# Optimization experiments

Hardware: AMD Instinct MI355X
Metric: run time of the kernel (lower is better)

The kernel has to match this reference:

```python
import jax, jax.numpy as jnp
import numpy as np

V_MIN = -10.0
V_MAX = 10.0
N_ATOMS = 101
LN_EPS = 1e-5

B = 131072
N_OBS = 60
N_ACT = 20
H = 256


def _layer_norm(x, g, b):
    mu = jnp.mean(x, axis=-1, keepdims=True)
    var = jnp.mean(jnp.square(x - mu), axis=-1, keepdims=True)
    return (x - mu) * jax.lax.rsqrt(var + LN_EPS) * g + b


def _mlp(x, W1, b1, g1, be1, W2, b2, g2, be2, W3, b3, g3, be3, W4, b4):
    h = jax.nn.silu(_layer_norm(x @ W1 + b1, g1, be1))
    h = jax.nn.silu(_layer_norm(h @ W2 + b2, g2, be2))
    h = jax.nn.silu(_layer_norm(h @ W3 + b3, g3, be3))
    return h @ W4 + b4  # [B, N_ATOMS] logits


def setup_inputs() -> dict:
    key = jax.random.key(0)
    ks = jax.random.split(key, 10)
    s = 0.05
    return {
        'obs': jax.random.normal(ks[0], (B, N_OBS), jnp.float32),
        'actions': jax.random.normal(ks[1], (B, N_ACT), jnp.float32),
        'rewards': jax.random.normal(ks[2], (B,), jnp.float32),
        'bootstrap': jax.random.uniform(ks[3], (B,), jnp.float32),
        'discount': jax.random.uniform(ks[4], (B,), jnp.float32, 0.95, 0.99),
        'q_support': jnp.linspace(V_MIN, V_MAX, N_ATOMS, dtype=jnp.float32),
        'W1': jax.random.normal(ks[5], (N_OBS + N_ACT, H), jnp.float32) * s,
        'b1': jnp.zeros((H,), jnp.float32),
        'g1': jnp.ones((H,), jnp.float32),
        'be1': jnp.zeros((H,), jnp.float32),
        'W2': jax.random.normal(ks[6], (H, H // 2), jnp.float32) * s,
        'b2': jnp.zeros((H // 2,), jnp.float32),
        'g2': jnp.ones((H // 2,), jnp.float32),
        'be2': jnp.zeros((H // 2,), jnp.float32),
        'W3': jax.random.normal(ks[7], (H // 2, H // 4), jnp.float32) * s,
        'b3': jnp.zeros((H // 4,), jnp.float32),
        'g3': jnp.ones((H // 4,), jnp.float32),
        'be3': jnp.zeros((H // 4,), jnp.float32),
        'W4': jax.random.normal(ks[8], (H // 4, N_ATOMS), jnp.float32) * s,
        'b4': jnp.zeros((N_ATOMS,), jnp.float32),
    }


def reference(obs, actions, rewards, bootstrap, discount, q_support,
              W1, b1, g1, be1, W2, b2, g2, be2, W3, b3, g3, be3, W4, b4):
    batch = rewards.shape[0]
    delta_z = (V_MAX - V_MIN) / (N_ATOMS - 1)
    # Bellman target support: [B, N_ATOMS]
    target_z = rewards[:, None] + bootstrap[:, None] * discount[:, None] * q_support
    target_z = jnp.clip(target_z, V_MIN, V_MAX)
    b = (target_z - V_MIN) / delta_z
    li = jnp.floor(b).astype(jnp.int32)
    ui = jnp.ceil(b).astype(jnp.int32)
    is_int = ui == li
    lower_mask = is_int & (li > 0)
    upper_mask = is_int & (li == 0)
    li = jnp.where(lower_mask, li - 1, li)
    ui = jnp.where(upper_mask, ui + 1, ui)
    lf = li.astype(b.dtype)
    uf = ui.astype(b.dtype)

    x = jnp.concatenate([obs, actions], axis=-1)
    logits = _mlp(x, W1, b1, g1, be1, W2, b2, g2, be2, W3, b3, g3, be3, W4, b4)
    next_dist = jax.nn.softmax(logits, axis=1)

    size = batch * N_ATOMS
    offset = (jnp.arange(batch, dtype=jnp.int32) * N_ATOMS)[:, None]
    l_idx = jnp.clip((li + offset).reshape(-1), 0, size - 1)
    u_idx = jnp.clip((ui + offset).reshape(-1), 0, size - 1)
    lw = (next_dist * (uf - b)).reshape(-1)
    uw = (next_dist * (b - lf)).reshape(-1)
    proj = jnp.zeros((size,), next_dist.dtype).at[l_idx].add(lw).at[u_idx].add(uw)
    return proj.reshape(batch, N_ATOMS)
```

## Files before the change

### kernel.cpp

```cpp
#include <hip/hip_runtime.h>
#include <math.h>

typedef __bf16 bf16x8 __attribute__((ext_vector_type(8)));
typedef float f32x4 __attribute__((ext_vector_type(4)));

__global__ void conv_weights(const float* __restrict__ W1, const float* __restrict__ W2,
                             const float* __restrict__ W3, const float* __restrict__ W4,
                             __bf16* __restrict__ ws)
{
  const int f = blockIdx.x;
  const int lane = threadIdx.x;
  int f0, ntot, Ksrc, Nsrc, off;
  const float* W;
  if (f < 48)       { f0 = f;       ntot = 16; Ksrc = 80;  Nsrc = 256; W = W1; off = 0; }
  else if (f < 112) { f0 = f - 48;  ntot = 8;  Ksrc = 256; Nsrc = 128; W = W2; off = 24576; }
  else if (f < 128) { f0 = f - 112; ntot = 4;  Ksrc = 128; Nsrc = 64;  W = W3; off = 57344; }
  else              { f0 = f - 128; ntot = 8;  Ksrc = 64;  Nsrc = 101; W = W4; off = 65536; }
  const int kt = f0 / ntot, nt = f0 % ntot;
  const int q = lane >> 4, c = lane & 15;
  const int n = nt * 16 + c;
  bf16x8 v;
#pragma unroll
  for (int j = 0; j < 8; ++j) {
    const int k = kt * 32 + q * 8 + j;
    const float x = (k < Ksrc && n < Nsrc) ? W[k * Nsrc + n] : 0.f;
    v[j] = (__bf16)x;
  }
  ((bf16x8*)(ws + off))[f0 * 64 + lane] = v;
}


template<int KT, int NTW, int NTOT, int SIN, int SOUT>
__device__ __forceinline__ void layer(
    const __bf16* __restrict__ aIn, __bf16* __restrict__ aOut,
    const bf16x8* __restrict__ Bfrags, int n0t,
    const float* __restrict__ bias, const float* __restrict__ g,
    const float* __restrict__ be,
    float* __restrict__ lnS, float* __restrict__ lnS2,
    float* __restrict__ muS, float* __restrict__ rsS,
    int t, int lane)
{
  const int q = lane >> 4, c = lane & 15;
  const int wv = t >> 6;
  bf16x8 Bf[KT][NTW];
#pragma unroll
  for (int kt = 0; kt < KT; ++kt)
#pragma unroll
    for (int nt = 0; nt < NTW; ++nt)
      Bf[kt][nt] = Bfrags[(kt * NTOT + n0t + nt) * 64 + lane];
  f32x4 acc[2][NTW];
#pragma unroll
  for (int nt = 0; nt < NTW; ++nt) {
    const float bb = bias[(n0t + nt) * 16 + c];
    f32x4 v = {bb, bb, bb, bb};
    acc[0][nt] = v;
    acc[1][nt] = v;
  }
#pragma unroll
  for (int mt = 0; mt < 2; ++mt)
#pragma unroll
    for (int kt = 0; kt < KT; ++kt) {
      const bf16x8 A = *(const bf16x8*)(aIn + (mt * 16 + c) * SIN + kt * 32 + q * 8);
#pragma unroll
      for (int nt = 0; nt < NTW; ++nt)
        acc[mt][nt] = __builtin_amdgcn_mfma_f32_16x16x32_bf16(A, Bf[kt][nt], acc[mt][nt], 0, 0, 0);
    }
#pragma unroll
  for (int mt = 0; mt < 2; ++mt)
#pragma unroll
    for (int r = 0; r < 4; ++r) {
      float s = 0.f, s2 = 0.f;
#pragma unroll
      for (int nt = 0; nt < NTW; ++nt) { const float v = acc[mt][nt][r]; s += v; s2 += v * v; }
      s += __shfl_xor(s, 1); s2 += __shfl_xor(s2, 1);
      s += __shfl_xor(s, 2); s2 += __shfl_xor(s2, 2);
      s += __shfl_xor(s, 4); s2 += __shfl_xor(s2, 4);
      s += __shfl_xor(s, 8); s2 += __shfl_xor(s2, 8);
      if (c == 0) {
        const int row = mt * 16 + 4 * q + r;
        lnS[row * 4 + wv] = s;
        lnS2[row * 4 + wv] = s2;
      }
    }
  __syncthreads();
  if (t < 32) {
    const float s  = lnS[t * 4] + lnS[t * 4 + 1] + lnS[t * 4 + 2] + lnS[t * 4 + 3];
    const float s2 = lnS2[t * 4] + lnS2[t * 4 + 1] + lnS2[t * 4 + 2] + lnS2[t * 4 + 3];
    const float invN = 1.f / (float)(NTOT * 16);
    const float mu = s * invN;
    const float var = s2 * invN - mu * mu;
    muS[t] = mu;
    rsS[t] = rsqrtf(var + 1e-5f);
  }
  __syncthreads();
#pragma unroll
  for (int nt = 0; nt < NTW; ++nt) {
    const int col = (n0t + nt) * 16 + c;
    const float gg = g[col], bb = be[col];
#pragma unroll
    for (int mt = 0; mt < 2; ++mt)
#pragma unroll
      for (int r = 0; r < 4; ++r) {
        const int row = mt * 16 + 4 * q + r;
        float v = (acc[mt][nt][r] - muS[row]) * rsS[row] * gg + bb;
        v = v / (1.f + __expf(-v));
        aOut[row * SOUT + col] = (__bf16)v;
      }
  }
  __syncthreads();
}

__global__ __launch_bounds__(256, 4)
void sacq_mfma(const float* __restrict__ obs,  const float* __restrict__ act,
               const float* __restrict__ rew,  const float* __restrict__ boot,
               const float* __restrict__ disc, const float* __restrict__ qsup,
               const float* __restrict__ b1, const float* __restrict__ g1, const float* __restrict__ be1,
               const float* __restrict__ b2, const float* __restrict__ g2, const float* __restrict__ be2,
               const float* __restrict__ b3, const float* __restrict__ g3, const float* __restrict__ be3,
               const float* __restrict__ b4,
               const __bf16* __restrict__ ws,
               float* __restrict__ out)
{
  __shared__ float smf[7152];
  __bf16* xb = (__bf16*)smf;
  __bf16* h2 = (__bf16*)smf;
  __bf16* h1 = (__bf16*)(smf + 2176);
  __bf16* h3 = (__bf16*)(smf + 2176);
  float* proj = smf + 3328;
  float* lnS  = smf + 6656;
  float* lnS2 = smf + 6784;
  float* muS  = smf + 6912;
  float* rsS  = smf + 6944;
  float* qsL  = smf + 6976;
  float* rwL  = smf + 7080;
  float* bdL  = smf + 7112;

  const int t = threadIdx.x;
  const int lane = t & 63, wv = t >> 6;
  const int q = lane >> 4, c = lane & 15;
  const long row0 = (long)blockIdx.x * 32;

  for (int idx = t; idx < 32 * 60; idx += 256) {
    const int r = idx / 60, cc = idx - r * 60;
    xb[r * 104 + cc] = (__bf16)obs[row0 * 60 + idx];
  }
  for (int idx = t; idx < 32 * 20; idx += 256) {
    const int r = idx / 20, cc = idx - r * 20;
    xb[r * 104 + 60 + cc] = (__bf16)act[row0 * 20 + idx];
  }
  for (int idx = t; idx < 32 * 24; idx += 256) {
    const int r = idx / 24, cc = idx - r * 24;
    xb[r * 104 + 80 + cc] = (__bf16)0.f;
  }
  if (t < 101) qsL[t] = qsup[t];
  if (t >= 128 && t < 160) {
    const int r = t - 128;
    rwL[r] = rew[row0 + r];
    bdL[r] = boot[row0 + r] * disc[row0 + r];
  }
  __syncthreads();

  const bf16x8* wsf = (const bf16x8*)ws;
  layer<3, 4, 16, 104, 264>(xb, h1, wsf + 0,    wv * 4, b1, g1, be1, lnS, lnS2, muS, rsS, t, lane);
  layer<8, 2, 8, 264, 136>(h1, h2, wsf + 3072, wv * 2, b2, g2, be2, lnS, lnS2, muS, rsS, t, lane);
  layer<4, 1, 4, 136, 72>(h2, h3, wsf + 7168,  wv,     b3, g3, be3, lnS, lnS2, muS, rsS, t, lane);

  {
    const int mtw = wv >> 1;
    const int half = wv & 1;
    bf16x8 Bf4[2][4];
#pragma unroll
    for (int kt = 0; kt < 2; ++kt)
#pragma unroll
      for (int nt = 0; nt < 4; ++nt)
        Bf4[kt][nt] = wsf[8192 + (kt * 8 + half * 4 + nt) * 64 + lane];
    f32x4 a4[4];
#pragma unroll
    for (int nt = 0; nt < 4; ++nt) {
      const int col = (half * 4 + nt) * 16 + c;
      const float bb = (col < 101) ? b4[col] : 0.f;
      f32x4 v = {bb, bb, bb, bb};
      a4[nt] = v;
    }
#pragma unroll
    for (int kt = 0; kt < 2; ++kt) {
      const bf16x8 A = *(const bf16x8*)(h3 + (mtw * 16 + c) * 72 + kt * 32 + q * 8);
#pragma unroll
      for (int nt = 0; nt < 4; ++nt)
        a4[nt] = __builtin_amdgcn_mfma_f32_16x16x32_bf16(A, Bf4[kt][nt], a4[nt], 0, 0, 0);
    }
#pragma unroll
    for (int r = 0; r < 4; ++r) {
      float mx = -3.4e38f;
#pragma unroll
      for (int nt = 0; nt < 4; ++nt) {
        const int col = (half * 4 + nt) * 16 + c;
        if (col < 101) mx = fmaxf(mx, a4[nt][r]);
      }
      mx = fmaxf(mx, __shfl_xor(mx, 1));
      mx = fmaxf(mx, __shfl_xor(mx, 2));
      mx = fmaxf(mx, __shfl_xor(mx, 4));
      mx = fmaxf(mx, __shfl_xor(mx, 8));
      if (c == 0) lnS[(mtw * 16 + 4 * q + r) * 2 + half] = mx;
    }
    __syncthreads();
    for (int idx = t; idx < 32 * 104; idx += 256) proj[idx] = 0.f;
#pragma unroll
    for (int r = 0; r < 4; ++r) {
      const int row = mtw * 16 + 4 * q + r;
      const float mxf = fmaxf(lnS[row * 2], lnS[row * 2 + 1]);
      float s = 0.f;
#pragma unroll
      for (int nt = 0; nt < 4; ++nt) {
        const int col = (half * 4 + nt) * 16 + c;
        const float e = (col < 101) ? __expf(a4[nt][r] - mxf) : 0.f;
        a4[nt][r] = e;
        s += e;
      }
      s += __shfl_xor(s, 1);
      s += __shfl_xor(s, 2);
      s += __shfl_xor(s, 4);
      s += __shfl_xor(s, 8);
      if (c == 0) lnS2[row * 2 + half] = s;
    }
    __syncthreads();
#pragma unroll
    for (int r = 0; r < 4; ++r) {
      const int row = mtw * 16 + 4 * q + r;
      const float inv = 1.f / (lnS2[row * 2] + lnS2[row * 2 + 1]);
      const float rw = rwL[row], bd = bdL[row];
#pragma unroll
      for (int nt = 0; nt < 4; ++nt) {
        const int col = (half * 4 + nt) * 16 + c;
        if (col < 101) {
          const float p = a4[nt][r] * inv;
          float tz = rw + bd * qsL[col];
          tz = fminf(fmaxf(tz, -10.f), 10.f);
          const float b_ = (tz + 10.f) / 0.2f;
          const float fl = floorf(b_), cl = ceilf(b_);
          int li = (int)fl, ui = (int)cl;
          if (ui == li) { if (li > 0) --li; else ++ui; }
          atomicAdd(&proj[row * 104 + li], p * ((float)ui - b_));
          atomicAdd(&proj[row * 104 + ui], p * (b_ - (float)li));
        }
      }
    }
    __syncthreads();
  }

  for (int idx = t; idx < 32 * 101; idx += 256) {
    const int r = idx / 101, cc = idx - r * 101;
    out[row0 * 101 + idx] = proj[r * 104 + cc];
  }
}

extern "C" void kernel_launch(void* const* d_in, const int* in_sizes, int n_in,
                              void* d_out, int out_size, void* d_ws, size_t ws_size,
                              hipStream_t stream)
{
  const int B = in_sizes[2];
  __bf16* ws = (__bf16*)d_ws;

  conv_weights<<<dim3(144), dim3(64), 0, stream>>>(
      (const float*)d_in[6], (const float*)d_in[10], (const float*)d_in[14],
      (const float*)d_in[18], ws);

  sacq_mfma<<<dim3(B / 32), dim3(256), 0, stream>>>(
      (const float*)d_in[0],  (const float*)d_in[1],  (const float*)d_in[2],
      (const float*)d_in[3],  (const float*)d_in[4],  (const float*)d_in[5],
      (const float*)d_in[7],  (const float*)d_in[8],  (const float*)d_in[9],
      (const float*)d_in[11], (const float*)d_in[12], (const float*)d_in[13],
      (const float*)d_in[15], (const float*)d_in[16], (const float*)d_in[17],
      (const float*)d_in[19], ws, (float*)d_out);
}
```

Before: 356.8 us.

## Make each wavefront own 16 rows end-to-end, removing block-wide syncs

Restructures the fused MLP+projection kernel so each wavefront handles 16 batch rows through all four layers independently, using private LDS regions and wave-level shuffles for LayerNorm and softmax instead of cross-wave reductions and __syncthreads. Weights are read from global (cache) per MFMA instead of preloaded fragments, inputs are loaded straight into registers, and output is written with vector stores. This removes barrier stalls and cross-wave LDS reductions. In exchange it needs more registers (launch bounds drop to 3 blocks per SIMD), more LDS per block, and heavier weight traffic per wave.

```diff
diff --git a/kernel.cpp b/kernel.cpp
--- a/kernel.cpp
+++ b/kernel.cpp
@@ -8,8 +8,8 @@
                              const float* __restrict__ W3, const float* __restrict__ W4,
                              __bf16* __restrict__ ws)
 {
-  const int f = blockIdx.x;
-  const int lane = threadIdx.x;
+  const int f = blockIdx.x * 4 + (threadIdx.x >> 6);
+  const int lane = threadIdx.x & 63;
   int f0, ntot, Ksrc, Nsrc, off;
   const float* W;
   if (f < 48)       { f0 = f;       ntot = 16; Ksrc = 80;  Nsrc = 256; W = W1; off = 0; }
@@ -30,88 +30,8 @@
 }
 
 
-template<int KT, int NTW, int NTOT, int SIN, int SOUT>
-__device__ __forceinline__ void layer(
-    const __bf16* __restrict__ aIn, __bf16* __restrict__ aOut,
-    const bf16x8* __restrict__ Bfrags, int n0t,
-    const float* __restrict__ bias, const float* __restrict__ g,
-    const float* __restrict__ be,
-    float* __restrict__ lnS, float* __restrict__ lnS2,
-    float* __restrict__ muS, float* __restrict__ rsS,
-    int t, int lane)
-{
-  const int q = lane >> 4, c = lane & 15;
-  const int wv = t >> 6;
-  bf16x8 Bf[KT][NTW];
-#pragma unroll
-  for (int kt = 0; kt < KT; ++kt)
-#pragma unroll
-    for (int nt = 0; nt < NTW; ++nt)
-      Bf[kt][nt] = Bfrags[(kt * NTOT + n0t + nt) * 64 + lane];
-  f32x4 acc[2][NTW];
-#pragma unroll
-  for (int nt = 0; nt < NTW; ++nt) {
-    const float bb = bias[(n0t + nt) * 16 + c];
-    f32x4 v = {bb, bb, bb, bb};
-    acc[0][nt] = v;
-    acc[1][nt] = v;
-  }
-#pragma unroll
-  for (int mt = 0; mt < 2; ++mt)
-#pragma unroll
-    for (int kt = 0; kt < KT; ++kt) {
-      const bf16x8 A = *(const bf16x8*)(aIn + (mt * 16 + c) * SIN + kt * 32 + q * 8);
-#pragma unroll
-      for (int nt = 0; nt < NTW; ++nt)
-        acc[mt][nt] = __builtin_amdgcn_mfma_f32_16x16x32_bf16(A, Bf[kt][nt], acc[mt][nt], 0, 0, 0);
-    }
-#pragma unroll
-  for (int mt = 0; mt < 2; ++mt)
-#pragma unroll
-    for (int r = 0; r < 4; ++r) {
-      float s = 0.f, s2 = 0.f;
-#pragma unroll
-      for (int nt = 0; nt < NTW; ++nt) { const float v = acc[mt][nt][r]; s += v; s2 += v * v; }
-      s += __shfl_xor(s, 1); s2 += __shfl_xor(s2, 1);
-      s += __shfl_xor(s, 2); s2 += __shfl_xor(s2, 2);
-      s += __shfl_xor(s, 4); s2 += __shfl_xor(s2, 4);
-      s += __shfl_xor(s, 8); s2 += __shfl_xor(s2, 8);
-      if (c == 0) {
-        const int row = mt * 16 + 4 * q + r;
-        lnS[row * 4 + wv] = s;
-        lnS2[row * 4 + wv] = s2;
-      }
-    }
-  __syncthreads();
-  if (t < 32) {
-    const float s  = lnS[t * 4] + lnS[t * 4 + 1] + lnS[t * 4 + 2] + lnS[t * 4 + 3];
-    const float s2 = lnS2[t * 4] + lnS2[t * 4 + 1] + lnS2[t * 4 + 2] + lnS2[t * 4 + 3];
-    const float invN = 1.f / (float)(NTOT * 16);
-    const float mu = s * invN;
-    const float var = s2 * invN - mu * mu;
-    muS[t] = mu;
-    rsS[t] = rsqrtf(var + 1e-5f);
-  }
-  __syncthreads();
-#pragma unroll
-  for (int nt = 0; nt < NTW; ++nt) {
-    const int col = (n0t + nt) * 16 + c;
-    const float gg = g[col], bb = be[col];
-#pragma unroll
-    for (int mt = 0; mt < 2; ++mt)
-#pragma unroll
-      for (int r = 0; r < 4; ++r) {
-        const int row = mt * 16 + 4 * q + r;
-        float v = (acc[mt][nt][r] - muS[row]) * rsS[row] * gg + bb;
-        v = v / (1.f + __expf(-v));
-        aOut[row * SOUT + col] = (__bf16)v;
-      }
-  }
-  __syncthreads();
-}
-
-__global__ __launch_bounds__(256, 4)
-void sacq_mfma(const float* __restrict__ obs,  const float* __restrict__ act,
+__global__ __launch_bounds__(256, 3)
+void sacq_wave(const float* __restrict__ obs,  const float* __restrict__ act,
                const float* __restrict__ rew,  const float* __restrict__ boot,
                const float* __restrict__ disc, const float* __restrict__ qsup,
                const float* __restrict__ b1, const float* __restrict__ g1, const float* __restrict__ be1,
@@ -121,136 +41,250 @@
                const __bf16* __restrict__ ws,
                float* __restrict__ out)
 {
-  __shared__ float smf[7152];
-  __bf16* xb = (__bf16*)smf;
-  __bf16* h2 = (__bf16*)smf;
-  __bf16* h1 = (__bf16*)(smf + 2176);
-  __bf16* h3 = (__bf16*)(smf + 2176);
-  float* proj = smf + 3328;
-  float* lnS  = smf + 6656;
-  float* lnS2 = smf + 6784;
-  float* muS  = smf + 6912;
-  float* rsS  = smf + 6944;
-  float* qsL  = smf + 6976;
-  float* rwL  = smf + 7080;
-  float* bdL  = smf + 7112;
-
+  __shared__ float sm[13120];
   const int t = threadIdx.x;
-  const int lane = t & 63, wv = t >> 6;
+  const int wv = t >> 6, lane = t & 63;
   const int q = lane >> 4, c = lane & 15;
-  const long row0 = (long)blockIdx.x * 32;
-
-  for (int idx = t; idx < 32 * 60; idx += 256) {
-    const int r = idx / 60, cc = idx - r * 60;
-    xb[r * 104 + cc] = (__bf16)obs[row0 * 60 + idx];
-  }
-  for (int idx = t; idx < 32 * 20; idx += 256) {
-    const int r = idx / 20, cc = idx - r * 20;
-    xb[r * 104 + 60 + cc] = (__bf16)act[row0 * 20 + idx];
-  }
-  for (int idx = t; idx < 32 * 24; idx += 256) {
-    const int r = idx / 24, cc = idx - r * 24;
-    xb[r * 104 + 80 + cc] = (__bf16)0.f;
-  }
-  if (t < 101) qsL[t] = qsup[t];
-  if (t >= 128 && t < 160) {
-    const int r = t - 128;
-    rwL[r] = rew[row0 + r];
-    bdL[r] = boot[row0 + r] * disc[row0 + r];
-  }
-  __syncthreads();
-
+  float* smw = sm + wv * 3280;
+  __bf16* h1 = (__bf16*)smw;
+  __bf16* h2 = (__bf16*)(smw + 2192);
+  __bf16* h3 = (__bf16*)smw;
+  float*  proj = smw + 576;
+  const int row0w = blockIdx.x * 64 + wv * 16;
   const bf16x8* wsf = (const bf16x8*)ws;
-  layer<3, 4, 16, 104, 264>(xb, h1, wsf + 0,    wv * 4, b1, g1, be1, lnS, lnS2, muS, rsS, t, lane);
-  layer<8, 2, 8, 264, 136>(h1, h2, wsf + 3072, wv * 2, b2, g2, be2, lnS, lnS2, muS, rsS, t, lane);
-  layer<4, 1, 4, 136, 72>(h2, h3, wsf + 7168,  wv,     b3, g3, be3, lnS, lnS2, muS, rsS, t, lane);
-
-  {
-    const int mtw = wv >> 1;
-    const int half = wv & 1;
-    bf16x8 Bf4[2][4];
-#pragma unroll
-    for (int kt = 0; kt < 2; ++kt)
+
+  {
+    bf16x8 A1[3];
+    const float* obsR = obs + (size_t)(row0w + c) * 60;
+    const float* actR = act + (size_t)(row0w + c) * 20;
+#pragma unroll
+    for (int kt = 0; kt < 3; ++kt)
+#pragma unroll
+      for (int j = 0; j < 8; ++j) {
+        const int k = kt * 32 + q * 8 + j;
+        float xv = 0.f;
+        if (k < 60) xv = obsR[k];
+        else if (k < 80) xv = actR[k - 60];
+        A1[kt][j] = (__bf16)xv;
+      }
+    f32x4 acc1[16];
+#pragma unroll
+    for (int nt = 0; nt < 16; ++nt) {
+      const float bb = b1[nt * 16 + c];
+      f32x4 v = {bb, bb, bb, bb};
+      acc1[nt] = v;
+    }
+#pragma unroll
+    for (int kt = 0; kt < 3; ++kt)
+#pragma unroll
+      for (int nt = 0; nt < 16; ++nt)
+        acc1[nt] = __builtin_amdgcn_mfma_f32_16x16x32_bf16(A1[kt], wsf[(kt * 16 + nt) * 64 + lane], acc1[nt], 0, 0, 0);
+
+    float mu[4], rs[4];
+#pragma unroll
+    for (int r = 0; r < 4; ++r) {
+      float s = 0.f, s2 = 0.f;
+#pragma unroll
+      for (int nt = 0; nt < 16; ++nt) { const float v = acc1[nt][r]; s += v; s2 += v * v; }
+      s += __shfl_xor(s, 1); s2 += __shfl_xor(s2, 1);
+      s += __shfl_xor(s, 2); s2 += __shfl_xor(s2, 2);
+      s += __shfl_xor(s, 4); s2 += __shfl_xor(s2, 4);
+      s += __shfl_xor(s, 8); s2 += __shfl_xor(s2, 8);
+      const float m = s * (1.f / 256.f);
+      mu[r] = m;
+      rs[r] = rsqrtf(s2 * (1.f / 256.f) - m * m + 1e-5f);
+    }
+#pragma unroll
+    for (int nt = 0; nt < 16; ++nt) {
+      const int col = nt * 16 + c;
+      const float gg = g1[col], bb = be1[col];
+#pragma unroll
+      for (int r = 0; r < 4; ++r) {
+        float v = (acc1[nt][r] - mu[r]) * rs[r] * gg + bb;
+        v = v * __builtin_amdgcn_rcpf(1.f + __expf(-v));
+        h1[(4 * q + r) * 264 + col] = (__bf16)v;
+      }
+    }
+  }
+
+  {
+    f32x4 acc2[8];
+#pragma unroll
+    for (int nt = 0; nt < 8; ++nt) {
+      const float bb = b2[nt * 16 + c];
+      f32x4 v = {bb, bb, bb, bb};
+      acc2[nt] = v;
+    }
+#pragma unroll
+    for (int kt = 0; kt < 8; ++kt) {
+      const bf16x8 A2 = *(const bf16x8*)(h1 + c * 264 + kt * 32 + q * 8);
+#pragma unroll
+      for (int nt = 0; nt < 8; ++nt)
+        acc2[nt] = __builtin_amdgcn_mfma_f32_16x16x32_bf16(A2, wsf[3072 + (kt * 8 + nt) * 64 + lane], acc2[nt], 0, 0, 0);
+    }
+    float mu[4], rs[4];
+#pragma unroll
+    for (int r = 0; r < 4; ++r) {
+      float s = 0.f, s2 = 0.f;
+#pragma unroll
+      for (int nt = 0; nt < 8; ++nt) { const float v = acc2[nt][r]; s += v; s2 += v * v; }
+      s += __shfl_xor(s, 1); s2 += __shfl_xor(s2, 1);
+      s += __shfl_xor(s, 2); s2 += __shfl_xor(s2, 2);
+      s += __shfl_xor(s, 4); s2 += __shfl_xor(s2, 4);
+      s += __shfl_xor(s, 8); s2 += __shfl_xor(s2, 8);
+      const float m = s * (1.f / 128.f);
+      mu[r] = m;
+      rs[r] = rsqrtf(s2 * (1.f / 128.f) - m * m + 1e-5f);
+    }
+#pragma unroll
+    for (int nt = 0; nt < 8; ++nt) {
+      const int col = nt * 16 + c;
+      const float gg = g2[col], bb = be2[col];
+#pragma unroll
+      for (int r = 0; r < 4; ++r) {
+        float v = (acc2[nt][r] - mu[r]) * rs[r] * gg + bb;
+        v = v * __builtin_amdgcn_rcpf(1.f + __expf(-v));
+        h2[(4 * q + r) * 136 + col] = (__bf16)v;
+      }
+    }
+  }
+
+  {
+    f32x4 acc3[4];
+#pragma unroll
+    for (int nt = 0; nt < 4; ++nt) {
+      const float bb = b3[nt * 16 + c];
+      f32x4 v = {bb, bb, bb, bb};
+      acc3[nt] = v;
+    }
+#pragma unroll
+    for (int kt = 0; kt < 4; ++kt) {
+      const bf16x8 A3 = *(const bf16x8*)(h2 + c * 136 + kt * 32 + q * 8);
 #pragma unroll
       for (int nt = 0; nt < 4; ++nt)
-        Bf4[kt][nt] = wsf[8192 + (kt * 8 + half * 4 + nt) * 64 + lane];
-    f32x4 a4[4];
+        acc3[nt] = __builtin_amdgcn_mfma_f32_16x16x32_bf16(A3, wsf[7168 + (kt * 4 + nt) * 64 + lane], acc3[nt], 0, 0, 0);
+    }
+    float mu[4], rs[4];
+#pragma unroll
+    for (int r = 0; r < 4; ++r) {
+      float s = 0.f, s2 = 0.f;
+#pragma unroll
+      for (int nt = 0; nt < 4; ++nt) { const float v = acc3[nt][r]; s += v; s2 += v * v; }
+      s += __shfl_xor(s, 1); s2 += __shfl_xor(s2, 1);
+      s += __shfl_xor(s, 2); s2 += __shfl_xor(s2, 2);
+      s += __shfl_xor(s, 4); s2 += __shfl_xor(s2, 4);
+      s += __shfl_xor(s, 8); s2 += __shfl_xor(s2, 8);
+      const float m = s * (1.f / 64.f);
+      mu[r] = m;
+      rs[r] = rsqrtf(s2 * (1.f / 64.f) - m * m + 1e-5f);
+    }
 #pragma unroll
     for (int nt = 0; nt < 4; ++nt) {
-      const int col = (half * 4 + nt) * 16 + c;
+      const int col = nt * 16 + c;
+      const float gg = g3[col], bb = be3[col];
+#pragma unroll
+      for (int r = 0; r < 4; ++r) {
+        float v = (acc3[nt][r] - mu[r]) * rs[r] * gg + bb;
+        v = v * __builtin_amdgcn_rcpf(1.f + __expf(-v));
+        h3[(4 * q + r) * 72 + col] = (__bf16)v;
+      }
+    }
+  }
+
+  {
+    f32x4 a4[7];
+#pragma unroll
+    for (int nt = 0; nt < 7; ++nt) {
+      const int col = nt * 16 + c;
       const float bb = (col < 101) ? b4[col] : 0.f;
       f32x4 v = {bb, bb, bb, bb};
       a4[nt] = v;
     }
 #pragma unroll
     for (int kt = 0; kt < 2; ++kt) {
-      const bf16x8 A = *(const bf16x8*)(h3 + (mtw * 16 + c) * 72 + kt * 32 + q * 8);
-#pragma unroll
-      for (int nt = 0; nt < 4; ++nt)
-        a4[nt] = __builtin_amdgcn_mfma_f32_16x16x32_bf16(A, Bf4[kt][nt], a4[nt], 0, 0, 0);
-    }
-#pragma unroll
-    for (int r = 0; r < 4; ++r) {
-      float mx = -3.4e38f;
-#pragma unroll
-      for (int nt = 0; nt < 4; ++nt) {
-        const int col = (half * 4 + nt) * 16 + c;
-        if (col < 101) mx = fmaxf(mx, a4[nt][r]);
-      }
-      mx = fmaxf(mx, __shfl_xor(mx, 1));
-      mx = fmaxf(mx, __shfl_xor(mx, 2));
-      mx = fmaxf(mx, __shfl_xor(mx, 4));
-      mx = fmaxf(mx, __shfl_xor(mx, 8));
-      if (c == 0) lnS[(mtw * 16 + 4 * q + r) * 2 + half] = mx;
-    }
-    __syncthreads();
-    for (int idx = t; idx < 32 * 104; idx += 256) proj[idx] = 0.f;
-#pragma unroll
-    for (int r = 0; r < 4; ++r) {
-      const int row = mtw * 16 + 4 * q + r;
-      const float mxf = fmaxf(lnS[row * 2], lnS[row * 2 + 1]);
-      float s = 0.f;
-#pragma unroll
-      for (int nt = 0; nt < 4; ++nt) {
-        const int col = (half * 4 + nt) * 16 + c;
-        const float e = (col < 101) ? __expf(a4[nt][r] - mxf) : 0.f;
+      const bf16x8 A4 = *(const bf16x8*)(h3 + c * 72 + kt * 32 + q * 8);
+#pragma unroll
+      for (int nt = 0; nt < 7; ++nt)
+        a4[nt] = __builtin_amdgcn_mfma_f32_16x16x32_bf16(A4, wsf[8192 + (kt * 8 + nt) * 64 + lane], a4[nt], 0, 0, 0);
+    }
+
+    {
+      f32x4 z = {0.f, 0.f, 0.f, 0.f};
+      f32x4* p4 = (f32x4*)proj;
+      for (int i = lane; i < 404; i += 64) p4[i] = z;
+    }
+
+    float mx4[4] = {-3.4e38f, -3.4e38f, -3.4e38f, -3.4e38f};
+#pragma unroll
+    for (int nt = 0; nt < 7; ++nt) {
+      const bool ok = (nt < 6) | (c < 5);
+#pragma unroll
+      for (int r = 0; r < 4; ++r)
+        if (ok) mx4[r] = fmaxf(mx4[r], a4[nt][r]);
+    }
+#pragma unroll
+    for (int r = 0; r < 4; ++r) {
+      mx4[r] = fmaxf(mx4[r], __shfl_xor(mx4[r], 1));
+      mx4[r] = fmaxf(mx4[r], __shfl_xor(mx4[r], 2));
+      mx4[r] = fmaxf(mx4[r], __shfl_xor(mx4[r], 4));
+      mx4[r] = fmaxf(mx4[r], __shfl_xor(mx4[r], 8));
+    }
+    float sm4[4] = {0.f, 0.f, 0.f, 0.f};
+#pragma unroll
+    for (int nt = 0; nt < 7; ++nt) {
+      const bool ok = (nt < 6) | (c < 5);
+#pragma unroll
+      for (int r = 0; r < 4; ++r) {
+        const float e = ok ? __expf(a4[nt][r] - mx4[r]) : 0.f;
         a4[nt][r] = e;
-        s += e;
-      }
+        sm4[r] += e;
+      }
+    }
+    float inv4[4];
+#pragma unroll
+    for (int r = 0; r < 4; ++r) {
+      float s = sm4[r];
       s += __shfl_xor(s, 1);
       s += __shfl_xor(s, 2);
       s += __shfl_xor(s, 4);
       s += __shfl_xor(s, 8);
-      if (c == 0) lnS2[row * 2 + half] = s;
-    }
-    __syncthreads();
-#pragma unroll
-    for (int r = 0; r < 4; ++r) {
-      const int row = mtw * 16 + 4 * q + r;
-      const float inv = 1.f / (lnS2[row * 2] + lnS2[row * 2 + 1]);
-      const float rw = rwL[row], bd = bdL[row];
-#pragma unroll
-      for (int nt = 0; nt < 4; ++nt) {
-        const int col = (half * 4 + nt) * 16 + c;
-        if (col < 101) {
-          const float p = a4[nt][r] * inv;
-          float tz = rw + bd * qsL[col];
+      inv4[r] = __builtin_amdgcn_rcpf(s);
+    }
+
+    float rwv[4], bdv[4];
+#pragma unroll
+    for (int r = 0; r < 4; ++r) {
+      const int gr = row0w + 4 * q + r;
+      rwv[r] = rew[gr];
+      bdv[r] = boot[gr] * disc[gr];
+    }
+
+#pragma unroll
+    for (int nt = 0; nt < 7; ++nt) {
+      const int col = nt * 16 + c;
+      if ((nt < 6) | (c < 5)) {
+        const float qsv = qsup[col];
+#pragma unroll
+        for (int r = 0; r < 4; ++r) {
+          const float p = a4[nt][r] * inv4[r];
+          float tz = rwv[r] + bdv[r] * qsv;
           tz = fminf(fmaxf(tz, -10.f), 10.f);
-          const float b_ = (tz + 10.f) / 0.2f;
+          const float b_ = (tz + 10.f) * 5.f;
           const float fl = floorf(b_), cl = ceilf(b_);
           int li = (int)fl, ui = (int)cl;
           if (ui == li) { if (li > 0) --li; else ++ui; }
-          atomicAdd(&proj[row * 104 + li], p * ((float)ui - b_));
-          atomicAdd(&proj[row * 104 + ui], p * (b_ - (float)li));
+          const int rb = (4 * q + r) * 101;
+          atomicAdd(&proj[rb + li], p * ((float)ui - b_));
+          atomicAdd(&proj[rb + ui], p * (b_ - (float)li));
         }
       }
     }
-    __syncthreads();
-  }
-
-  for (int idx = t; idx < 32 * 101; idx += 256) {
-    const int r = idx / 101, cc = idx - r * 101;
-    out[row0 * 101 + idx] = proj[r * 104 + cc];
+  }
+
+  {
+    const f32x4* p4 = (const f32x4*)proj;
+    f32x4* o4 = (f32x4*)(out + (size_t)row0w * 101);
+    for (int i = lane; i < 404; i += 64) o4[i] = p4[i];
   }
 }
 
@@ -261,11 +295,11 @@
   const int B = in_sizes[2];
   __bf16* ws = (__bf16*)d_ws;
 
-  conv_weights<<<dim3(144), dim3(64), 0, stream>>>(
+  conv_weights<<<dim3(36), dim3(256), 0, stream>>>(
       (const float*)d_in[6], (const float*)d_in[10], (const float*)d_in[14],
       (const float*)d_in[18], ws);
 
-  sacq_mfma<<<dim3(B / 32), dim3(256), 0, stream>>>(
+  sacq_wave<<<dim3(B / 64), dim3(256), 0, stream>>>(
       (const float*)d_in[0],  (const float*)d_in[1],  (const float*)d_in[2],
       (const float*)d_in[3],  (const float*)d_in[4],  (const float*)d_in[5],
       (const float*)d_in[7],  (const float*)d_in[8],  (const float*)d_in[9],
```

New measurement: 334.0 us. 1.07x faster.
